# Kernel tuning notes

Hardware: AMD Instinct MI355X
Metric: run time of the kernel (lower is better)

The kernel has to match this reference:

```python
import jax, jax.numpy as jnp
import numpy as np

NHEAD = 16
D_MODEL = 1024
D_K = D_MODEL // NHEAD


def setup_inputs() -> dict:
    key = jax.random.key(0)
    ks = jax.random.split(key, 12)
    B, S, D = 2, 2048, D_MODEL
    scale = 1.0 / np.sqrt(D)
    inp = {
        "value": jax.random.normal(ks[0], (B, S, D), dtype=jnp.float32),
        "key": jax.random.normal(ks[1], (B, S, D), dtype=jnp.float32),
        "query": jax.random.normal(ks[2], (B, S, D), dtype=jnp.float32),
        "mask": jax.random.randint(ks[3], (B, 1, S, S), 0, 2, dtype=jnp.int32),
        "Wv": jax.random.normal(ks[4], (D, D), dtype=jnp.float32) * scale,
        "bv": jnp.zeros((D,), dtype=jnp.float32),
        "Wk": jax.random.normal(ks[5], (D, D), dtype=jnp.float32) * scale,
        "bk": jnp.zeros((D,), dtype=jnp.float32),
        "Wq": jax.random.normal(ks[6], (D, D), dtype=jnp.float32) * scale,
        "bq": jnp.zeros((D,), dtype=jnp.float32),
        "Wo": jax.random.normal(ks[7], (D, D), dtype=jnp.float32) * scale,
        "bo": jnp.zeros((D,), dtype=jnp.float32),
    }
    return inp


def reference(value, key, query, mask, Wv, bv, Wk, bk, Wq, bq, Wo, bo):
    B, S, D = value.shape
    H, Dk = NHEAD, D_K

    def proj(x, W, b):
        # nn.Linear: x @ W^T + b, then split heads -> [B, H, S, Dk]
        return (x @ W.T + b).reshape(B, S, H, Dk).transpose(0, 2, 1, 3)

    v = proj(value, Wv, bv)
    k = proj(key, Wk, bk)
    q = proj(query, Wq, bq)

    # NOTE: source code swaps K and V when calling attention():
    #   scores = Q @ V^T / sqrt(d_k);  out = softmax(scores) @ K
    scores = jnp.einsum("bhqd,bhkd->bhqk", q, v) / jnp.sqrt(jnp.float32(Dk))
    scores = jnp.where(mask == 0, jnp.float32(-1e9), scores)
    attn = jax.nn.softmax(scores, axis=-1)  # [B, H, S, S]
    attr_value = jnp.einsum("bhqk,bhkd->bhqd", attn, k)

    out = attr_value.transpose(0, 2, 1, 3).reshape(B, S, H * Dk)
    return out @ Wo.T + bo
```

## Files before the change

### kernel.cpp

```cpp
#include <hip/hip_runtime.h>

#define S_LEN 2048
#define DMODEL 1024
#define NHEADS 16
#define DKH 64

typedef __attribute__((ext_vector_type(8))) short bf16x8;
typedef __attribute__((ext_vector_type(4))) float f32x4;

#if __has_builtin(__builtin_amdgcn_exp2f)
#define EXP2F(x) __builtin_amdgcn_exp2f(x)
#define QSCALE (0.125f * 1.44269504f)
#else
#define EXP2F(x) __expf(x)
#define QSCALE 0.125f
#endif

static __device__ __forceinline__ short f2bf(float f) {
    unsigned b = __float_as_uint(f);
    b = (b + 0x7FFFu + ((b >> 16) & 1u)) >> 16;
    return (short)b;
}

static __device__ __forceinline__ unsigned pktrunc(float lo, float hi) {
#if __has_builtin(__builtin_amdgcn_perm)
    return __builtin_amdgcn_perm(__float_as_uint(hi), __float_as_uint(lo), 0x07060302u);
#else
    return (__float_as_uint(lo) >> 16) | (__float_as_uint(hi) & 0xFFFF0000u);
#endif
}

static __device__ __forceinline__ f32x4 mfma16(bf16x8 a, bf16x8 b, f32x4 c) {
    return __builtin_amdgcn_mfma_f32_16x16x32_bf16(a, b, c, 0, 0, 0);
}

static __device__ __forceinline__ void glds16(const short* g, short* l) {
    __builtin_amdgcn_global_load_lds(
        (const __attribute__((address_space(1))) void*)g,
        (__attribute__((address_space(3))) void*)l, 16, 0, 0);
}

struct CvtArgs { const float* src[7]; short* dst[7]; };

__global__ __launch_bounds__(256) void prep(CvtArgs a, const int* __restrict__ mask,
                                            unsigned long long* __restrict__ mw) {
    if (blockIdx.x < 8192) {
        const size_t i8 = ((size_t)blockIdx.x * 256 + threadIdx.x) * 8;
        int seg; size_t off;
        if (i8 < ((size_t)12 << 20)) { seg = (int)(i8 >> 22); off = i8 & ((1u << 22) - 1); }
        else { size_t r = i8 - ((size_t)12 << 20); seg = 3 + (int)(r >> 20); off = r & ((1u << 20) - 1); }
        const float* s = a.src[seg] + off;
        float4 x0 = *(const float4*)s, x1 = *(const float4*)(s + 4);
        short o[8];
        o[0] = f2bf(x0.x); o[1] = f2bf(x0.y); o[2] = f2bf(x0.z); o[3] = f2bf(x0.w);
        o[4] = f2bf(x1.x); o[5] = f2bf(x1.y); o[6] = f2bf(x1.z); o[7] = f2bf(x1.w);
        *(uint4*)(a.dst[seg] + off) = *(uint4*)o;
    } else {
        const int wv = ((blockIdx.x - 8192) << 2) + (threadIdx.x >> 6);
        const int lane = threadIdx.x & 63;
        const size_t base = (size_t)wv << 4;
        #pragma unroll 4
        for (int it = 0; it < 16; ++it) {
            const size_t w = base + it;
            const int m = mask[(w << 6) + lane];
            unsigned long long bal = __ballot(m != 0);
            if (lane == 0) mw[w] = bal;
        }
    }
}

struct GemmArgs { const short* X[3]; const short* W[3]; const float* B[3];
                  void* C[3]; float scale[3]; };

template <int MODE>
__global__ __launch_bounds__(256) void gemm_bt(GemmArgs a) {
    __shared__ short Ah[128 * 32];
    __shared__ short Bh[128 * 32];
    const int z = blockIdx.z;
    const short* X = a.X[z];
    const short* W = a.W[z];
    const float* bias = a.B[z];
    const float scl = a.scale[z];

    const int t = threadIdx.x, wid = t >> 6, lane = t & 63;
    const int l15 = lane & 15, lq = lane >> 4;
    const int m0 = blockIdx.x << 7, n0 = blockIdx.y << 7;
    const int wm = (wid >> 1) << 6, wn = (wid & 1) << 6;

    const int kb = (lane & 3) ^ ((lane >> 3) & 3);
    const int r0 = (wid << 5) + (lane >> 2);
    const short* ag0 = X + (size_t)(m0 + r0) * 1024 + (kb << 3);
    const short* ag1 = ag0 + 16 * 1024;
    const short* bg0 = W + (size_t)(n0 + r0) * 1024 + (kb << 3);
    const short* bg1 = bg0 + 16 * 1024;
    short* lA0 = Ah + (wid << 5) * 32;
    short* lA1 = lA0 + 16 * 32;
    short* lB0 = Bh + (wid << 5) * 32;
    short* lB1 = lB0 + 16 * 32;

    const int fpos = (lq ^ ((l15 >> 1) & 3)) << 3;

    f32x4 acc[4][4] = {};

    for (int k0 = 0; k0 < 1024; k0 += 32) {
        __syncthreads();
        glds16(ag0, lA0); glds16(ag1, lA1);
        glds16(bg0, lB0); glds16(bg1, lB1);
        ag0 += 32; ag1 += 32; bg0 += 32; bg1 += 32;
        __syncthreads();

        bf16x8 af[4], bfr[4];
        #pragma unroll
        for (int i = 0; i < 4; ++i)
            af[i] = *(const bf16x8*)&Ah[(wm + i * 16 + l15) * 32 + fpos];
        #pragma unroll
        for (int j = 0; j < 4; ++j)
            bfr[j] = *(const bf16x8*)&Bh[(wn + j * 16 + l15) * 32 + fpos];
        #pragma unroll
        for (int i = 0; i < 4; ++i)
            #pragma unroll
            for (int j = 0; j < 4; ++j)
                acc[i][j] = mfma16(af[i], bfr[j], acc[i][j]);
    }

    #pragma unroll
    for (int j = 0; j < 4; ++j) {
        const int n = n0 + wn + j * 16 + l15;
        const float bn = bias[n];
        #pragma unroll
        for (int i = 0; i < 4; ++i) {
            const int mbase = m0 + wm + i * 16 + (lq << 2);
            #pragma unroll
            for (int r = 0; r < 4; ++r) {
                const float val = (acc[i][j][r] + bn) * scl;
                const int m = mbase + r;
                if (MODE == 0) {
                    const int b = m >> 11, s = m & 2047, h = n >> 6, d = n & 63;
                    ((short*)a.C[z])[((((size_t)(b * 16 + h)) << 11) + s) * 64 + d] = f2bf(val);
                } else {
                    ((float*)a.C[z])[((size_t)m << 10) + n] = val;
                }
            }
        }
    }
}

__global__ __launch_bounds__(256) void ktr(const short* __restrict__ kh,
                                           short* __restrict__ kt) {
    __shared__ short Ls[64 * 68];
    const int t = threadIdx.x;
    const int s0 = blockIdx.x << 6, bh = blockIdx.y;
    {
        const int r = t >> 2, cb = (t & 3) << 4;
        const short* src = kh + ((size_t)bh * 2048 + s0 + r) * 64 + cb;
        *(uint4*)&Ls[r * 68 + cb + 0] = *(const uint4*)src;
        *(uint4*)&Ls[r * 68 + cb + 8] = *(const uint4*)(src + 8);
    }
    __syncthreads();
    const int d = t >> 2, c0 = (t & 3) << 4;
    short ov[16];
    #pragma unroll
    for (int e = 0; e < 16; ++e) {
        const int c = c0 + e;
        const int jl = ((c & 3) << 4) | (c >> 2);
        ov[e] = Ls[jl * 68 + d];
    }
    short* dst = kt + ((size_t)bh * 64 + d) * 2048 + s0 + c0;
    *(uint4*)(dst + 0) = *(uint4*)(ov + 0);
    *(uint4*)(dst + 8) = *(uint4*)(ov + 8);
}

__global__ __launch_bounds__(256, 4) void attn3(
    const short* __restrict__ Qh, const short* __restrict__ Vh,
    const short* __restrict__ Kt, const unsigned long long* __restrict__ MW,
    short* __restrict__ Opart, float* __restrict__ lpart)
{
    __shared__ short Vs[64 * 64];
    __shared__ short Ks[64 * 64];
    __shared__ short Ps[128 * 64];

    const int t = threadIdx.x, wid = t >> 6, lane = t & 63;
    const int l15 = lane & 15, lq = lane >> 4;
    const int bh = blockIdx.y, b = bh >> 4;
    const int z = blockIdx.z;
    const int q0 = blockIdx.x << 7;
    const int rowb = q0 + (wid << 5);
    const int jbase = z << 10;

    bf16x8 qf[2][2];
    #pragma unroll
    for (int mt = 0; mt < 2; ++mt) {
        const short* qp = Qh + ((size_t)bh * 2048 + rowb + mt * 16 + l15) * 64 + (lq << 3);
        qf[mt][0] = *(const bf16x8*)qp;
        qf[mt][1] = *(const bf16x8*)(qp + 32);
    }

    const int sr8 = lane >> 3;
    const int sc8 = (lane & 7) ^ sr8;
    const int wr = wid << 4;
    const short* vsrc = Vh + (size_t)bh * 131072 + (size_t)(jbase + wr + sr8) * 64 + (sc8 << 3);
    const short* ksrc = Kt + (size_t)bh * 131072 + (size_t)(wr + sr8) * 2048 + jbase + (sc8 << 3);
    short* vdst = Vs + (wr << 6);
    short* kdst = Ks + (wr << 6);

    const unsigned long long* mwp = MW + ((size_t)b * 2048 + rowb) * 32 + (z << 4);

    const int x7 = l15 & 7;
    const int off0 = ((lq ^ x7) << 3);
    const int off1 = (((4 | lq) ^ x7) << 3);

    float rsum[2][4] = {};
    f32x4 O[2][4] = {};

    for (int jc = 0; jc < 16; ++jc) {
        __syncthreads();
        glds16(vsrc, vdst);
        glds16(vsrc + 512, vdst + 512);
        glds16(ksrc, kdst);
        glds16(ksrc + 8 * 2048, kdst + 512);
        vsrc += 64 * 64; ksrc += 64;

        uint2 mwv[2][4];
        #pragma unroll
        for (int mt = 0; mt < 2; ++mt)
            #pragma unroll
            for (int r = 0; r < 4; ++r)
                mwv[mt][r] = *(const uint2*)(mwp + (size_t)(mt * 16 + (lq << 2) + r) * 32 + jc);
        __syncthreads();

        bf16x8 vf[4][2];
        #pragma unroll
        for (int nt = 0; nt < 4; ++nt) {
            const short* vp = &Vs[((nt << 4) + l15) << 6];
            vf[nt][0] = *(const bf16x8*)(vp + off0);
            vf[nt][1] = *(const bf16x8*)(vp + off1);
        }

        #pragma unroll
        for (int mt = 0; mt < 2; ++mt) {
            f32x4 sc[4];
            #pragma unroll
            for (int nt = 0; nt < 4; ++nt) {
                f32x4 c = {};
                c = mfma16(qf[mt][0], vf[nt][0], c);
                c = mfma16(qf[mt][1], vf[nt][1], c);
                sc[nt] = c;
            }
            #pragma unroll
            for (int r = 0; r < 4; ++r) {
                float p[4];
                #pragma unroll
                for (int nt = 0; nt < 4; ++nt) {
                    const unsigned sel = (nt < 2) ? mwv[mt][r].x : mwv[mt][r].y;
                    const unsigned bit = (sel >> (((nt & 1) << 4) + l15)) & 1u;
                    const float e = EXP2F(sc[nt][r]);
                    p[nt] = bit ? e : 0.f;
                }
                const unsigned u01 = pktrunc(p[0], p[1]);
                const unsigned u23 = pktrunc(p[2], p[3]);
                rsum[mt][r] += __uint_as_float(u01 << 16) + __uint_as_float(u01 & 0xFFFF0000u)
                             + __uint_as_float(u23 << 16) + __uint_as_float(u23 & 0xFFFF0000u);
                const int row7 = ((lq << 2) + r) & 7;
                const int pcw = (l15 >> 1) ^ row7;
                uint2 pw; pw.x = u01; pw.y = u23;
                *(uint2*)&Ps[(((wid << 5) + (mt << 4) + (lq << 2) + r) << 6)
                             + (pcw << 3) + ((l15 & 1) << 2)] = pw;
            }
        }

        bf16x8 kf[4][2];
        #pragma unroll
        for (int nt = 0; nt < 4; ++nt) {
            const short* kp = &Ks[((nt << 4) + l15) << 6];
            kf[nt][0] = *(const bf16x8*)(kp + off0);
            kf[nt][1] = *(const bf16x8*)(kp + off1);
        }
        bf16x8 pf[2][2];
        #pragma unroll
        for (int mt = 0; mt < 2; ++mt) {
            const short* pp = &Ps[((wid << 5) + (mt << 4) + l15) << 6];
            pf[mt][0] = *(const bf16x8*)(pp + off0);
            pf[mt][1] = *(const bf16x8*)(pp + off1);
        }
        #pragma unroll
        for (int nt = 0; nt < 4; ++nt)
            #pragma unroll
            for (int mt = 0; mt < 2; ++mt) {
                O[mt][nt] = mfma16(pf[mt][0], kf[nt][0], O[mt][nt]);
                O[mt][nt] = mfma16(pf[mt][1], kf[nt][1], O[mt][nt]);
            }
    }

    const size_t zb = (size_t)(z * 32 + bh) * 2048;
    #pragma unroll
    for (int mt = 0; mt < 2; ++mt)
        #pragma unroll
        for (int r = 0; r < 4; ++r) {
            float s = rsum[mt][r];
            #pragma unroll
            for (int d = 1; d < 16; d <<= 1)
                s += __shfl_xor(s, d, 64);
            const int row = rowb + (mt << 4) + (lq << 2) + r;
            if (l15 == 0) lpart[zb + row] = s;
            #pragma unroll
            for (int nt = 0; nt < 4; ++nt)
                Opart[(zb + row) * 64 + (nt << 4) + l15] = f2bf(O[mt][nt][r]);
        }
}

__global__ __launch_bounds__(256) void combine(const short* __restrict__ Op,
                                               const float* __restrict__ lp,
                                               short* __restrict__ attr) {
    const int idx = blockIdx.x * 256 + threadIdx.x;
    const int d8 = (idx & 7) << 3;
    const int srow = (idx >> 3) & 2047;
    const int bh = idx >> 14, b = bh >> 4, h = bh & 15;
    const size_t r0 = (size_t)bh * 2048 + srow;
    const size_t r1 = r0 + (size_t)32 * 2048;
    const short* p0 = Op + r0 * 64 + d8;
    const short* p1 = Op + r1 * 64 + d8;
    uint4 a = *(const uint4*)p0;
    uint4 c = *(const uint4*)p1;
    const float inv = 1.f / (lp[r0] + lp[r1]);
    const unsigned* au = (const unsigned*)&a;
    const unsigned* cu = (const unsigned*)&c;
    short o[8];
    #pragma unroll
    for (int i = 0; i < 4; ++i) {
        const float a0 = __uint_as_float(au[i] << 16);
        const float a1 = __uint_as_float(au[i] & 0xFFFF0000u);
        const float c0 = __uint_as_float(cu[i] << 16);
        const float c1 = __uint_as_float(cu[i] & 0xFFFF0000u);
        o[2 * i + 0] = f2bf((a0 + c0) * inv);
        o[2 * i + 1] = f2bf((a1 + c1) * inv);
    }
    *(uint4*)&attr[((size_t)b * 2048 + srow) * 1024 + (h << 6) + d8] = *(uint4*)o;
}

extern "C" void kernel_launch(void* const* d_in, const int* in_sizes, int n_in,
                              void* d_out, int out_size, void* d_ws, size_t ws_size,
                              hipStream_t stream) {
    const float* value = (const float*)d_in[0];
    const float* key   = (const float*)d_in[1];
    const float* query = (const float*)d_in[2];
    const int*   mask  = (const int*)d_in[3];
    const float* bv = (const float*)d_in[5];
    const float* bk = (const float*)d_in[7];
    const float* bq = (const float*)d_in[9];
    const float* bo = (const float*)d_in[11];
    float* out = (float*)d_out;

    const size_t M1 = (size_t)1 << 20, M4 = (size_t)1 << 22;
    short* ws = (short*)d_ws;
    short* Xq = ws;
    short* Xk = ws + M4;
    short* Xv = ws + 2 * M4;
    short* Wc0 = ws + 3 * M4;
    short* Wc1 = Wc0 + M1;
    short* Wc2 = Wc1 + M1;
    short* Wc3 = Wc2 + M1;
    short* qh = ws + 4 * M4;
    short* kh = ws + 5 * M4;
    short* vh = ws + 6 * M4;
    short* kt = ws + 7 * M4;
    unsigned long long* maskw = (unsigned long long*)(ws + 8 * M4);
    short* attr = Xq;
    short* Opart = Xk;
    float* lpart = (float*)Wc0;

    CvtArgs cv;
    cv.src[0] = query; cv.dst[0] = Xq;
    cv.src[1] = key;   cv.dst[1] = Xk;
    cv.src[2] = value; cv.dst[2] = Xv;
    cv.src[3] = (const float*)d_in[8];  cv.dst[3] = Wc0;
    cv.src[4] = (const float*)d_in[6];  cv.dst[4] = Wc1;
    cv.src[5] = (const float*)d_in[4];  cv.dst[5] = Wc2;
    cv.src[6] = (const float*)d_in[10]; cv.dst[6] = Wc3;
    prep<<<10240, 256, 0, stream>>>(cv, mask, maskw);

    GemmArgs g1;
    g1.X[0] = Xq; g1.W[0] = Wc0; g1.B[0] = bq; g1.C[0] = qh; g1.scale[0] = QSCALE;
    g1.X[1] = Xk; g1.W[1] = Wc1; g1.B[1] = bk; g1.C[1] = kh; g1.scale[1] = 1.f;
    g1.X[2] = Xv; g1.W[2] = Wc2; g1.B[2] = bv; g1.C[2] = vh; g1.scale[2] = 1.f;
    gemm_bt<0><<<dim3(32, 8, 3), 256, 0, stream>>>(g1);

    ktr<<<dim3(32, 32), 256, 0, stream>>>(kh, kt);

    attn3<<<dim3(16, 32, 2), 256, 0, stream>>>(qh, vh, kt, maskw, Opart, lpart);

    combine<<<2048, 256, 0, stream>>>(Opart, lpart, attr);

    GemmArgs g2;
    g2.X[0] = attr; g2.W[0] = Wc3; g2.B[0] = bo; g2.C[0] = out; g2.scale[0] = 1.f;
    g2.X[1] = attr; g2.W[1] = Wc3; g2.B[1] = bo; g2.C[1] = out; g2.scale[1] = 1.f;
    g2.X[2] = attr; g2.W[2] = Wc3; g2.B[2] = bo; g2.C[2] = out; g2.scale[2] = 1.f;
    gemm_bt<1><<<dim3(32, 8, 1), 256, 0, stream>>>(g2);
}
```

Before: 279.7 us.

## Keep P in registers via transposed scores and emit K transposed from GEMM

The attention kernel now computes the transposed score tile (V·Q), so the exponentiated probabilities land directly in the register layout that a 16x16x16 MFMA needs as its A operand. This removes the shared-memory P buffer and its extra barrier traffic, and the row sums are now taken with an MFMA against a ones vector instead of shuffles. The K projection GEMM swaps its operands to write K already transposed, which removes the separate transpose kernel and one intermediate buffer. In exchange it uses more, smaller-K MFMAs, and the transposed GEMM epilogue writes with a larger stride.

```diff
diff --git a/kernel.cpp b/kernel.cpp
--- a/kernel.cpp
+++ b/kernel.cpp
@@ -6,6 +6,7 @@
 #define DKH 64
 
 typedef __attribute__((ext_vector_type(8))) short bf16x8;
+typedef __attribute__((ext_vector_type(4))) short bf16x4;
 typedef __attribute__((ext_vector_type(4))) float f32x4;
 
 #if __has_builtin(__builtin_amdgcn_exp2f)
@@ -32,6 +33,10 @@
 
 static __device__ __forceinline__ f32x4 mfma16(bf16x8 a, bf16x8 b, f32x4 c) {
     return __builtin_amdgcn_mfma_f32_16x16x32_bf16(a, b, c, 0, 0, 0);
+}
+
+static __device__ __forceinline__ f32x4 mfma_k16(bf16x4 a, bf16x4 b, f32x4 c) {
+    return __builtin_amdgcn_mfma_f32_16x16x16bf16_1k(a, b, c, 0, 0, 0);
 }
 
 static __device__ __forceinline__ void glds16(const short* g, short* l) {
@@ -84,7 +89,9 @@
 
     const int t = threadIdx.x, wid = t >> 6, lane = t & 63;
     const int l15 = lane & 15, lq = lane >> 4;
-    const int m0 = blockIdx.x << 7, n0 = blockIdx.y << 7;
+    int m0, n0;
+    if (MODE == 0 && z == 2) { m0 = blockIdx.y << 7; n0 = blockIdx.x << 7; }
+    else                     { m0 = blockIdx.x << 7; n0 = blockIdx.y << 7; }
     const int wm = (wid >> 1) << 6, wn = (wid & 1) << 6;
 
     const int kb = (lane & 3) ^ ((lane >> 3) & 3);
@@ -123,6 +130,26 @@
                 acc[i][j] = mfma16(af[i], bfr[j], acc[i][j]);
     }
 
+    if (MODE == 0 && z == 2) {
+        #pragma unroll
+        for (int i = 0; i < 4; ++i) {
+            #pragma unroll
+            for (int r = 0; r < 4; ++r) {
+                const int o = m0 + wm + i * 16 + (lq << 2) + r;
+                const float bo_ = bias[o];
+                const int h = o >> 6, d = o & 63;
+                #pragma unroll
+                for (int j = 0; j < 4; ++j) {
+                    const int n = n0 + wn + j * 16 + l15;
+                    const int bb = n >> 11, s = n & 2047;
+                    ((short*)a.C[2])[(((size_t)((bb * 16 + h) << 6) + d) << 11) + s] =
+                        f2bf(acc[i][j][r] + bo_);
+                }
+            }
+        }
+        return;
+    }
+
     #pragma unroll
     for (int j = 0; j < 4; ++j) {
         const int n = n0 + wn + j * 16 + l15;
@@ -145,72 +172,55 @@
     }
 }
 
-__global__ __launch_bounds__(256) void ktr(const short* __restrict__ kh,
-                                           short* __restrict__ kt) {
-    __shared__ short Ls[64 * 68];
-    const int t = threadIdx.x;
-    const int s0 = blockIdx.x << 6, bh = blockIdx.y;
-    {
-        const int r = t >> 2, cb = (t & 3) << 4;
-        const short* src = kh + ((size_t)bh * 2048 + s0 + r) * 64 + cb;
-        *(uint4*)&Ls[r * 68 + cb + 0] = *(const uint4*)src;
-        *(uint4*)&Ls[r * 68 + cb + 8] = *(const uint4*)(src + 8);
-    }
-    __syncthreads();
-    const int d = t >> 2, c0 = (t & 3) << 4;
-    short ov[16];
-    #pragma unroll
-    for (int e = 0; e < 16; ++e) {
-        const int c = c0 + e;
-        const int jl = ((c & 3) << 4) | (c >> 2);
-        ov[e] = Ls[jl * 68 + d];
-    }
-    short* dst = kt + ((size_t)bh * 64 + d) * 2048 + s0 + c0;
-    *(uint4*)(dst + 0) = *(uint4*)(ov + 0);
-    *(uint4*)(dst + 8) = *(uint4*)(ov + 8);
-}
-
-__global__ __launch_bounds__(256, 4) void attn3(
+__global__ __launch_bounds__(256, 4) void attn4(
     const short* __restrict__ Qh, const short* __restrict__ Vh,
     const short* __restrict__ Kt, const unsigned long long* __restrict__ MW,
     short* __restrict__ Opart, float* __restrict__ lpart)
 {
     __shared__ short Vs[64 * 64];
     __shared__ short Ks[64 * 64];
-    __shared__ short Ps[128 * 64];
 
     const int t = threadIdx.x, wid = t >> 6, lane = t & 63;
     const int l15 = lane & 15, lq = lane >> 4;
     const int bh = blockIdx.y, b = bh >> 4;
     const int z = blockIdx.z;
-    const int q0 = blockIdx.x << 7;
-    const int rowb = q0 + (wid << 5);
+    const int ib = (blockIdx.x << 7) + (wid << 5);
     const int jbase = z << 10;
 
     bf16x8 qf[2][2];
     #pragma unroll
-    for (int mt = 0; mt < 2; ++mt) {
-        const short* qp = Qh + ((size_t)bh * 2048 + rowb + mt * 16 + l15) * 64 + (lq << 3);
-        qf[mt][0] = *(const bf16x8*)qp;
-        qf[mt][1] = *(const bf16x8*)(qp + 32);
-    }
-
-    const int sr8 = lane >> 3;
-    const int sc8 = (lane & 7) ^ sr8;
+    for (int it = 0; it < 2; ++it) {
+        const short* qp = Qh + ((size_t)bh * 2048 + ib + it * 16 + l15) * 64 + (lq << 3);
+        qf[it][0] = *(const bf16x8*)qp;
+        qf[it][1] = *(const bf16x8*)(qp + 32);
+    }
+
+    const int sr = lane >> 3, pc = lane & 7;
+    const int lc = pc ^ sr;
     const int wr = wid << 4;
-    const short* vsrc = Vh + (size_t)bh * 131072 + (size_t)(jbase + wr + sr8) * 64 + (sc8 << 3);
-    const short* ksrc = Kt + (size_t)bh * 131072 + (size_t)(wr + sr8) * 2048 + jbase + (sc8 << 3);
+    const short* vsrc = Vh + (size_t)bh * 131072 + (size_t)(jbase + wr + sr) * 64 + (lc << 3);
+    const short* ksrc = Kt + (size_t)bh * 131072 + (size_t)(wr + sr) * 2048 + jbase + (lc << 3);
     short* vdst = Vs + (wr << 6);
     short* kdst = Ks + (wr << 6);
 
-    const unsigned long long* mwp = MW + ((size_t)b * 2048 + rowb) * 32 + (z << 4);
+    const unsigned long long* mwp0 = MW + ((size_t)b * 2048 + ib + l15) * 32 + (z << 4);
+    const unsigned long long* mwp1 = mwp0 + (size_t)16 * 32;
 
     const int x7 = l15 & 7;
-    const int off0 = ((lq ^ x7) << 3);
-    const int off1 = (((4 | lq) ^ x7) << 3);
-
-    float rsum[2][4] = {};
+    int voff[2], koff[4];
+    #pragma unroll
+    for (int p = 0; p < 2; ++p) voff[p] = (((p << 2) + lq) ^ x7) << 3;
+    #pragma unroll
+    for (int jt = 0; jt < 4; ++jt) {
+        const int c8 = (jt << 2) + lq;
+        koff[jt] = (((c8 >> 1) ^ x7) << 3) + ((c8 & 1) << 2);
+    }
+
     f32x4 O[2][4] = {};
+    f32x4 lsum[2] = {};
+    bf16x4 ones;
+    #pragma unroll
+    for (int e = 0; e < 4; ++e) ones[e] = (short)0x3F80;
 
     for (int jc = 0; jc < 16; ++jc) {
         __syncthreads();
@@ -218,94 +228,73 @@
         glds16(vsrc + 512, vdst + 512);
         glds16(ksrc, kdst);
         glds16(ksrc + 8 * 2048, kdst + 512);
-        vsrc += 64 * 64; ksrc += 64;
-
-        uint2 mwv[2][4];
-        #pragma unroll
-        for (int mt = 0; mt < 2; ++mt)
-            #pragma unroll
-            for (int r = 0; r < 4; ++r)
-                mwv[mt][r] = *(const uint2*)(mwp + (size_t)(mt * 16 + (lq << 2) + r) * 32 + jc);
+        vsrc += 4096; ksrc += 64;
+
+        uint2 mword[2];
+        mword[0] = *(const uint2*)(mwp0 + jc);
+        mword[1] = *(const uint2*)(mwp1 + jc);
         __syncthreads();
 
         bf16x8 vf[4][2];
         #pragma unroll
-        for (int nt = 0; nt < 4; ++nt) {
-            const short* vp = &Vs[((nt << 4) + l15) << 6];
-            vf[nt][0] = *(const bf16x8*)(vp + off0);
-            vf[nt][1] = *(const bf16x8*)(vp + off1);
-        }
-
-        #pragma unroll
-        for (int mt = 0; mt < 2; ++mt) {
-            f32x4 sc[4];
-            #pragma unroll
-            for (int nt = 0; nt < 4; ++nt) {
-                f32x4 c = {};
-                c = mfma16(qf[mt][0], vf[nt][0], c);
-                c = mfma16(qf[mt][1], vf[nt][1], c);
-                sc[nt] = c;
-            }
-            #pragma unroll
-            for (int r = 0; r < 4; ++r) {
+        for (int jt = 0; jt < 4; ++jt) {
+            const short* vp = &Vs[((jt << 4) + l15) << 6];
+            vf[jt][0] = *(const bf16x8*)(vp + voff[0]);
+            vf[jt][1] = *(const bf16x8*)(vp + voff[1]);
+        }
+
+        bf16x4 paf[2][4];
+        #pragma unroll
+        for (int it = 0; it < 2; ++it) {
+            const unsigned wx = mword[it].x, wy = mword[it].y;
+            #pragma unroll
+            for (int jt = 0; jt < 4; ++jt) {
+                f32x4 sc = {};
+                sc = mfma16(vf[jt][0], qf[it][0], sc);
+                sc = mfma16(vf[jt][1], qf[it][1], sc);
+                const unsigned w32 = (jt < 2) ? wx : wy;
                 float p[4];
                 #pragma unroll
-                for (int nt = 0; nt < 4; ++nt) {
-                    const unsigned sel = (nt < 2) ? mwv[mt][r].x : mwv[mt][r].y;
-                    const unsigned bit = (sel >> (((nt & 1) << 4) + l15)) & 1u;
-                    const float e = EXP2F(sc[nt][r]);
-                    p[nt] = bit ? e : 0.f;
+                for (int r = 0; r < 4; ++r) {
+                    const unsigned bit = (w32 >> (((jt & 1) << 4) + (lq << 2) + r)) & 1u;
+                    const float e = EXP2F(sc[r]);
+                    p[r] = bit ? e : 0.f;
                 }
-                const unsigned u01 = pktrunc(p[0], p[1]);
-                const unsigned u23 = pktrunc(p[2], p[3]);
-                rsum[mt][r] += __uint_as_float(u01 << 16) + __uint_as_float(u01 & 0xFFFF0000u)
-                             + __uint_as_float(u23 << 16) + __uint_as_float(u23 & 0xFFFF0000u);
-                const int row7 = ((lq << 2) + r) & 7;
-                const int pcw = (l15 >> 1) ^ row7;
-                uint2 pw; pw.x = u01; pw.y = u23;
-                *(uint2*)&Ps[(((wid << 5) + (mt << 4) + (lq << 2) + r) << 6)
-                             + (pcw << 3) + ((l15 & 1) << 2)] = pw;
+                uint2 uu;
+                uu.x = pktrunc(p[0], p[1]);
+                uu.y = pktrunc(p[2], p[3]);
+                paf[it][jt] = __builtin_bit_cast(bf16x4, uu);
+                lsum[it] = mfma_k16(paf[it][jt], ones, lsum[it]);
             }
         }
 
-        bf16x8 kf[4][2];
-        #pragma unroll
-        for (int nt = 0; nt < 4; ++nt) {
-            const short* kp = &Ks[((nt << 4) + l15) << 6];
-            kf[nt][0] = *(const bf16x8*)(kp + off0);
-            kf[nt][1] = *(const bf16x8*)(kp + off1);
-        }
-        bf16x8 pf[2][2];
-        #pragma unroll
-        for (int mt = 0; mt < 2; ++mt) {
-            const short* pp = &Ps[((wid << 5) + (mt << 4) + l15) << 6];
-            pf[mt][0] = *(const bf16x8*)(pp + off0);
-            pf[mt][1] = *(const bf16x8*)(pp + off1);
-        }
-        #pragma unroll
-        for (int nt = 0; nt < 4; ++nt)
-            #pragma unroll
-            for (int mt = 0; mt < 2; ++mt) {
-                O[mt][nt] = mfma16(pf[mt][0], kf[nt][0], O[mt][nt]);
-                O[mt][nt] = mfma16(pf[mt][1], kf[nt][1], O[mt][nt]);
+        #pragma unroll
+        for (int dt = 0; dt < 4; ++dt) {
+            const short* kp = &Ks[((dt << 4) + l15) << 6];
+            #pragma unroll
+            for (int jt = 0; jt < 4; ++jt) {
+                const bf16x4 kfv = *(const bf16x4*)(kp + koff[jt]);
+                O[0][dt] = mfma_k16(paf[0][jt], kfv, O[0][dt]);
+                O[1][dt] = mfma_k16(paf[1][jt], kfv, O[1][dt]);
             }
-    }
-
-    const size_t zb = (size_t)(z * 32 + bh) * 2048;
-    #pragma unroll
-    for (int mt = 0; mt < 2; ++mt)
-        #pragma unroll
-        for (int r = 0; r < 4; ++r) {
-            float s = rsum[mt][r];
-            #pragma unroll
-            for (int d = 1; d < 16; d <<= 1)
-                s += __shfl_xor(s, d, 64);
-            const int row = rowb + (mt << 4) + (lq << 2) + r;
-            if (l15 == 0) lpart[zb + row] = s;
-            #pragma unroll
-            for (int nt = 0; nt < 4; ++nt)
-                Opart[(zb + row) * 64 + (nt << 4) + l15] = f2bf(O[mt][nt][r]);
-        }
+        }
+    }
+
+    const size_t zb = (size_t)((z << 5) + bh) * 2048;
+    #pragma unroll
+    for (int it = 0; it < 2; ++it) {
+        const int rb = ib + (it << 4) + (lq << 2);
+        if (l15 == 0) {
+            #pragma unroll
+            for (int r = 0; r < 4; ++r)
+                lpart[zb + rb + r] = lsum[it][r];
+        }
+        #pragma unroll
+        for (int dt = 0; dt < 4; ++dt)
+            #pragma unroll
+            for (int r = 0; r < 4; ++r)
+                Opart[(zb + rb + r) * 64 + (dt << 4) + l15] = f2bf(O[it][dt][r]);
+    }
 }
 
 __global__ __launch_bounds__(256) void combine(const short* __restrict__ Op,
@@ -317,10 +306,8 @@
     const int bh = idx >> 14, b = bh >> 4, h = bh & 15;
     const size_t r0 = (size_t)bh * 2048 + srow;
     const size_t r1 = r0 + (size_t)32 * 2048;
-    const short* p0 = Op + r0 * 64 + d8;
-    const short* p1 = Op + r1 * 64 + d8;
-    uint4 a = *(const uint4*)p0;
-    uint4 c = *(const uint4*)p1;
+    uint4 a = *(const uint4*)(Op + r0 * 64 + d8);
+    uint4 c = *(const uint4*)(Op + r1 * 64 + d8);
     const float inv = 1.f / (lp[r0] + lp[r1]);
     const unsigned* au = (const unsigned*)&a;
     const unsigned* cu = (const unsigned*)&c;
@@ -360,10 +347,9 @@
     short* Wc2 = Wc1 + M1;
     short* Wc3 = Wc2 + M1;
     short* qh = ws + 4 * M4;
-    short* kh = ws + 5 * M4;
+    short* kt = ws + 5 * M4;
     short* vh = ws + 6 * M4;
-    short* kt = ws + 7 * M4;
-    unsigned long long* maskw = (unsigned long long*)(ws + 8 * M4);
+    unsigned long long* maskw = (unsigned long long*)(ws + 7 * M4);
     short* attr = Xq;
     short* Opart = Xk;
     float* lpart = (float*)Wc0;
@@ -379,14 +365,12 @@
     prep<<<10240, 256, 0, stream>>>(cv, mask, maskw);
 
     GemmArgs g1;
-    g1.X[0] = Xq; g1.W[0] = Wc0; g1.B[0] = bq; g1.C[0] = qh; g1.scale[0] = QSCALE;
-    g1.X[1] = Xk; g1.W[1] = Wc1; g1.B[1] = bk; g1.C[1] = kh; g1.scale[1] = 1.f;
-    g1.X[2] = Xv; g1.W[2] = Wc2; g1.B[2] = bv; g1.C[2] = vh; g1.scale[2] = 1.f;
+    g1.X[0] = Xq;  g1.W[0] = Wc0; g1.B[0] = bq; g1.C[0] = qh; g1.scale[0] = QSCALE;
+    g1.X[1] = Xv;  g1.W[1] = Wc2; g1.B[1] = bv; g1.C[1] = vh; g1.scale[1] = 1.f;
+    g1.X[2] = Wc1; g1.W[2] = Xk;  g1.B[2] = bk; g1.C[2] = kt; g1.scale[2] = 1.f;
     gemm_bt<0><<<dim3(32, 8, 3), 256, 0, stream>>>(g1);
 
-    ktr<<<dim3(32, 32), 256, 0, stream>>>(kh, kt);
-
-    attn3<<<dim3(16, 32, 2), 256, 0, stream>>>(qh, vh, kt, maskw, Opart, lpart);
+    attn4<<<dim3(16, 32, 2), 256, 0, stream>>>(qh, vh, kt, maskw, Opart, lpart);
 
     combine<<<2048, 256, 0, stream>>>(Opart, lpart, attr);
 
```

Measured after the change: 270.2 us. 3.4% less time.
